# Kernel tuning notes

Hardware: AMD Instinct MI355X
Metric: run time of the kernel (lower is better)

Reference implementation:

```python
import jax, jax.numpy as jnp
import numpy as np

B, S, D, H = 2, 2048, 2048, 16
HD = D // H          # head_dim = 128
FF = 8192            # intermediate_size
LN_EPS = 1e-05
BIT_EPS = 1e-05


def _rope_tables(seq_len, head_dim):
    inv_freq = 1.0 / (10000.0 ** (np.arange(0, head_dim, 2, dtype=np.float64) / head_dim))
    ang = np.arange(seq_len, dtype=np.float64)[:, None] * inv_freq[None, :]  # [S, HD/2]
    ang = np.concatenate([ang, ang], axis=-1)  # [S, HD]
    return jnp.asarray(np.cos(ang), jnp.float32), jnp.asarray(np.sin(ang), jnp.float32)


def setup_inputs() -> dict:
    key = jax.random.key(0)
    ks = jax.random.split(key, 9)
    hidden_states = jax.random.normal(ks[0], (B, S, D), jnp.float32)
    # causal additive mask [1, S, S]
    causal = jnp.tril(jnp.ones((S, S), bool))
    attention_mask = jnp.where(causal, 0.0, -1e9)[None].astype(jnp.float32)
    cos, sin = _rope_tables(S, HD)
    w = lambda k, o, i: jax.random.normal(k, (o, i), jnp.float32) * 0.02
    return {
        'hidden_states': hidden_states,
        'attention_mask': attention_mask,
        'cos': cos, 'sin': sin,
        'wq': w(ks[1], D, D), 'wk': w(ks[2], D, D),
        'wv': w(ks[3], D, D), 'wo': w(ks[4], D, D),
        'wg': w(ks[5], FF, D), 'wu': w(ks[6], FF, D), 'wd': w(ks[7], D, FF),
        'ln1_w': jnp.ones((D,), jnp.float32),
        'ln2_w': jnp.ones((D,), jnp.float32),
    }


def bitlinear(x, w):
    # ternarize: clamp(round(w / (mean|w| + eps)), -1, 1); int8 cast in torch
    # breaks grad through the ternary values -> stop_gradient here.
    scale = jnp.mean(jnp.abs(w))
    tern = jax.lax.stop_gradient(jnp.clip(jnp.round(w / (scale + BIT_EPS)), -1.0, 1.0))
    # dequant = ternary * mean|w|, then standard linear (x @ W^T)
    return jnp.einsum('bsi,oi->bso', x, tern * scale)


def rmsnorm(x, w, eps=LN_EPS):
    var = jnp.mean(jnp.square(x.astype(jnp.float32)), axis=-1, keepdims=True)
    return w * (x * jax.lax.rsqrt(var + eps))


def rotate_half(x):
    x1, x2 = jnp.split(x, 2, axis=-1)
    return jnp.concatenate([-x2, x1], axis=-1)


def apply_rope(q, k, cos, sin):
    # q, k: [B, S, D] -> per-head rope -> back to [B, S, D]
    qh = q.reshape(B, S, H, HD)
    kh = k.reshape(B, S, H, HD)
    c = cos[None, :, None, :]
    s = sin[None, :, None, :]
    qe = qh * c + rotate_half(qh) * s
    ke = kh * c + rotate_half(kh) * s
    return qe.reshape(B, S, D), ke.reshape(B, S, D)


def reference(hidden_states, attention_mask, cos, sin,
              wq, wk, wv, wo, wg, wu, wd, ln1_w, ln2_w):
    residual = hidden_states
    # --- attention block ---
    x = rmsnorm(hidden_states, ln1_w)
    q = bitlinear(x, wq)
    k = bitlinear(x, wk)
    v = bitlinear(x, wv)
    q, k = apply_rope(q, k, cos, sin)
    # NOTE: scores over FULL hidden dim (no head split), scaled by sqrt(head_dim),
    # exactly as in the original module.
    scores = jnp.einsum('bsd,btd->bst', q, k) / jnp.sqrt(jnp.float32(HD))
    scores = scores + attention_mask
    probs = jax.nn.softmax(scores, axis=-1)
    attn_out = jnp.einsum('bst,btd->bsd', probs, v)
    attn_out = bitlinear(attn_out, wo)
    h = residual + attn_out
    # --- MLP block ---
    residual = h
    y = rmsnorm(h, ln2_w)
    gated = bitlinear(y, wg) * bitlinear(y, wu)
    out = bitlinear(gated, wd)
    return residual + out
```

## Files before the change

### kernel.cpp

```cpp
#include <hip/hip_runtime.h>
#include <stdint.h>

#define DEV __device__ __forceinline__

typedef __attribute__((ext_vector_type(8))) short short8;
typedef __attribute__((ext_vector_type(8))) __bf16 bf16x8;
typedef __attribute__((ext_vector_type(4))) float f32x4;

DEV unsigned short f2bf(float f) {
  union { float f; unsigned int u; } v; v.f = f;
  unsigned int r = v.u + 0x7fffu + ((v.u >> 16) & 1u);
  return (unsigned short)(r >> 16);
}
DEV float bf2f(unsigned short h) {
  union { unsigned int u; float f; } v; v.u = ((unsigned int)h) << 16;
  return v.f;
}
DEV f32x4 mfma16(short8 a, short8 b, f32x4 c) {
  return __builtin_amdgcn_mfma_f32_16x16x32_bf16(
      __builtin_bit_cast(bf16x8, a), __builtin_bit_cast(bf16x8, b), c, 0, 0, 0);
}
DEV void gload_lds16(const void* g, void* lds) {
  __builtin_amdgcn_global_load_lds(
      (const __attribute__((address_space(1))) void*)g,
      (__attribute__((address_space(3))) void*)lds, 16, 0, 0);
}

struct MArgs {
  const float* src[7];
  unsigned short* dst[7];
  int n[7];
  int sidx[7];
};

__global__ __launch_bounds__(256) void absmean_partial_multi(
    MArgs a, float* __restrict__ partial) {
  const int m = blockIdx.y;
  const float4* w4 = (const float4*)a.src[m];
  const int n4 = a.n[m] >> 2;
  float s = 0.f;
  for (int i = blockIdx.x * 256 + threadIdx.x; i < n4; i += 1024 * 256) {
    float4 v = w4[i];
    s += fabsf(v.x) + fabsf(v.y) + fabsf(v.z) + fabsf(v.w);
  }
#pragma unroll
  for (int mm = 1; mm < 64; mm <<= 1) s += __shfl_xor(s, mm);
  __shared__ float red[4];
  if ((threadIdx.x & 63) == 0) red[threadIdx.x >> 6] = s;
  __syncthreads();
  if (threadIdx.x == 0)
    partial[m * 1024 + blockIdx.x] = red[0] + red[1] + red[2] + red[3];
}

__global__ __launch_bounds__(256) void absmean_final(
    const float* __restrict__ partial, float* __restrict__ scales) {
  __shared__ double red[256];
  const int m = blockIdx.x;
  double s = 0.0;
  for (int i = threadIdx.x; i < 1024; i += 256) s += (double)partial[m * 1024 + i];
  red[threadIdx.x] = s;
  __syncthreads();
  for (int t = 128; t > 0; t >>= 1) {
    if (threadIdx.x < t) red[threadIdx.x] += red[threadIdx.x + t];
    __syncthreads();
  }
  if (threadIdx.x == 0) {
    const long long cnt = (m < 4) ? 4194304ll : 16777216ll;
    scales[m] = (float)(red[0] / (double)cnt);
  }
}

__global__ __launch_bounds__(256) void quantize_multi(
    MArgs a, const float* __restrict__ scales) {
  const int m = blockIdx.y;
  const float sc = scales[a.sidx[m]];
  const float inv = 1.f / (sc + 1e-5f);
  const float4* src = (const float4*)a.src[m];
  ushort4* dst = (ushort4*)a.dst[m];
  const int n4 = a.n[m] >> 2;
  for (int i = blockIdx.x * 256 + threadIdx.x; i < n4; i += 2048 * 256) {
    float4 v = src[i];
    ushort4 o;
    o.x = f2bf(fminf(fmaxf(rintf(v.x * inv), -1.f), 1.f) * sc);
    o.y = f2bf(fminf(fmaxf(rintf(v.y * inv), -1.f), 1.f) * sc);
    o.z = f2bf(fminf(fmaxf(rintf(v.z * inv), -1.f), 1.f) * sc);
    o.w = f2bf(fminf(fmaxf(rintf(v.w * inv), -1.f), 1.f) * sc);
    dst[i] = o;
  }
}

__global__ __launch_bounds__(256) void rmsnorm_k(
    const float* __restrict__ x, const float* __restrict__ wt,
    unsigned short* __restrict__ out) {
  const long long t = blockIdx.x;
  const float* xr = x + t * 2048;
  const int i0 = threadIdx.x * 8;
  float4 a = *(const float4*)(xr + i0);
  float4 b = *(const float4*)(xr + i0 + 4);
  float ss = a.x * a.x + a.y * a.y + a.z * a.z + a.w * a.w +
             b.x * b.x + b.y * b.y + b.z * b.z + b.w * b.w;
#pragma unroll
  for (int m = 1; m < 64; m <<= 1) ss += __shfl_xor(ss, m);
  __shared__ float red[4];
  if ((threadIdx.x & 63) == 0) red[threadIdx.x >> 6] = ss;
  __syncthreads();
  float tot = red[0] + red[1] + red[2] + red[3];
  float rs = rsqrtf(tot * (1.f / 2048.f) + 1e-5f);
  float4 wa = *(const float4*)(wt + i0);
  float4 wb = *(const float4*)(wt + i0 + 4);
  ushort4 o1, o2;
  o1.x = f2bf(a.x * wa.x * rs); o1.y = f2bf(a.y * wa.y * rs);
  o1.z = f2bf(a.z * wa.z * rs); o1.w = f2bf(a.w * wa.w * rs);
  o2.x = f2bf(b.x * wb.x * rs); o2.y = f2bf(b.y * wb.y * rs);
  o2.z = f2bf(b.z * wb.z * rs); o2.w = f2bf(b.w * wb.w * rs);
  *(ushort4*)(out + t * 2048 + i0) = o1;
  *(ushort4*)(out + t * 2048 + i0 + 4) = o2;
}

__global__ __launch_bounds__(256) void combine_rms(
    const float* __restrict__ ep, const unsigned short* __restrict__ p,
    const float* __restrict__ wt, float* __restrict__ hout,
    unsigned short* __restrict__ yout) {
  const long long t = blockIdx.x;
  const int i0 = threadIdx.x * 8;
  const long long base = t * 2048 + i0;
  float4 e1 = *(const float4*)(ep + base);
  float4 e2 = *(const float4*)(ep + base + 4);
  short8 pa = *(const short8*)(p + base);
  short8 pb = *(const short8*)(p + 8388608 + base);
  const float e[8] = {e1.x, e1.y, e1.z, e1.w, e2.x, e2.y, e2.z, e2.w};
  float h[8];
#pragma unroll
  for (int i = 0; i < 8; ++i)
    h[i] = e[i] + bf2f((unsigned short)pa[i]) + bf2f((unsigned short)pb[i]);
  float4 h1 = {h[0], h[1], h[2], h[3]};
  float4 h2 = {h[4], h[5], h[6], h[7]};
  *(float4*)(hout + base) = h1;
  *(float4*)(hout + base + 4) = h2;
  float ss = 0.f;
#pragma unroll
  for (int i = 0; i < 8; ++i) ss += h[i] * h[i];
#pragma unroll
  for (int m = 1; m < 64; m <<= 1) ss += __shfl_xor(ss, m);
  __shared__ float red[4];
  if ((threadIdx.x & 63) == 0) red[threadIdx.x >> 6] = ss;
  __syncthreads();
  const float tot = red[0] + red[1] + red[2] + red[3];
  const float rs = rsqrtf(tot * (1.f / 2048.f) + 1e-5f);
  float4 wa = *(const float4*)(wt + i0);
  float4 wb = *(const float4*)(wt + i0 + 4);
  ushort4 o1, o2;
  o1.x = f2bf(h[0] * wa.x * rs); o1.y = f2bf(h[1] * wa.y * rs);
  o1.z = f2bf(h[2] * wa.z * rs); o1.w = f2bf(h[3] * wa.w * rs);
  o2.x = f2bf(h[4] * wb.x * rs); o2.y = f2bf(h[5] * wb.y * rs);
  o2.z = f2bf(h[6] * wb.z * rs); o2.w = f2bf(h[7] * wb.w * rs);
  *(ushort4*)(yout + base) = o1;
  *(ushort4*)(yout + base + 4) = o2;
}

__global__ __launch_bounds__(256) void combine2(
    const float* __restrict__ ep, const unsigned short* __restrict__ p,
    float* __restrict__ out) {
  const long long base = (long long)blockIdx.x * 2048 + threadIdx.x * 8;
  float4 e1 = *(const float4*)(ep + base);
  float4 e2 = *(const float4*)(ep + base + 4);
  short8 pa = *(const short8*)(p + base);
  short8 pb = *(const short8*)(p + 8388608 + base);
  float4 o1, o2;
  o1.x = e1.x + bf2f((unsigned short)pa[0]) + bf2f((unsigned short)pb[0]);
  o1.y = e1.y + bf2f((unsigned short)pa[1]) + bf2f((unsigned short)pb[1]);
  o1.z = e1.z + bf2f((unsigned short)pa[2]) + bf2f((unsigned short)pb[2]);
  o1.w = e1.w + bf2f((unsigned short)pa[3]) + bf2f((unsigned short)pb[3]);
  o2.x = e2.x + bf2f((unsigned short)pa[4]) + bf2f((unsigned short)pb[4]);
  o2.y = e2.y + bf2f((unsigned short)pa[5]) + bf2f((unsigned short)pb[5]);
  o2.z = e2.z + bf2f((unsigned short)pa[6]) + bf2f((unsigned short)pb[6]);
  o2.w = e2.w + bf2f((unsigned short)pa[7]) + bf2f((unsigned short)pb[7]);
  *(float4*)(out + base) = o1;
  *(float4*)(out + base + 4) = o2;
}

__global__ __launch_bounds__(256) void rope_k(
    const unsigned short* __restrict__ qkv, const float* __restrict__ cosT,
    const float* __restrict__ sinT, unsigned short* __restrict__ qr,
    unsigned short* __restrict__ kr) {
  const long long gid = (long long)blockIdx.x * 256 + threadIdx.x;
  const int t = (int)(gid >> 10);
  const int r = (int)(gid & 1023);
  const int h = r >> 6, d = r & 63;
  const int s = t & 2047;
  const unsigned short* row = qkv + (long long)t * 6144;
  const float c = cosT[s * 128 + d], sn = sinT[s * 128 + d];
  const int col = h * 128 + d;
  const float SC = 0.08838834764831845f;
  float q1 = bf2f(row[col]), q2 = bf2f(row[col + 64]);
  float k1 = bf2f(row[2048 + col]), k2 = bf2f(row[2048 + col + 64]);
  long long ob = (long long)t * 2048 + col;
  qr[ob] = f2bf((q1 * c - q2 * sn) * SC);
  qr[ob + 64] = f2bf((q2 * c + q1 * sn) * SC);
  kr[ob] = f2bf(k1 * c - k2 * sn);
  kr[ob + 64] = f2bf(k2 * c + k1 * sn);
}

__global__ __launch_bounds__(256) void vtrans_k(
    const unsigned short* __restrict__ qkv, unsigned short* __restrict__ vt) {
  __shared__ unsigned short tile[64][66];
  const int tt = blockIdx.x << 6, dd = blockIdx.y << 6;
  const long long b = blockIdx.z;
  const int r0 = threadIdx.x >> 4, c0 = (threadIdx.x & 15) << 2;
#pragma unroll
  for (int i = 0; i < 4; ++i) {
    const int row = r0 + i * 16;
    ushort4 v = *(const ushort4*)&qkv[(b * 2048 + tt + row) * 6144 + 4096 + dd + c0];
    tile[row][c0] = v.x; tile[row][c0 + 1] = v.y;
    tile[row][c0 + 2] = v.z; tile[row][c0 + 3] = v.w;
  }
  __syncthreads();
#pragma unroll
  for (int i = 0; i < 4; ++i) {
    const int d = r0 + i * 16;
    ushort4 o;
    o.x = tile[c0][d]; o.y = tile[c0 + 1][d];
    o.z = tile[c0 + 2][d]; o.w = tile[c0 + 3][d];
    *(ushort4*)&vt[(b * 2048 + dd + d) * 2048 + tt + c0] = o;
  }
}

__global__ __launch_bounds__(256) void softmax_causal(
    const float* __restrict__ scores, unsigned short* __restrict__ probs) {
  const int r = blockIdx.x;
  const int s = r & 2047;
  const float* src = scores + (long long)r * 2048;
  unsigned short* dst = probs + (long long)r * 2048;
  const int L = s + 1;
  const int j0 = threadIdx.x * 8;
  float4 a = *(const float4*)(src + j0);
  float4 b = *(const float4*)(src + j0 + 4);
  float v[8] = {a.x, a.y, a.z, a.w, b.x, b.y, b.z, b.w};
  float mx = -1e30f;
#pragma unroll
  for (int i = 0; i < 8; ++i) {
    if (j0 + i >= L) v[i] = -1e30f;
    mx = fmaxf(mx, v[i]);
  }
#pragma unroll
  for (int m = 1; m < 64; m <<= 1) mx = fmaxf(mx, __shfl_xor(mx, m));
  __shared__ float redM[4], redS[4];
  if ((threadIdx.x & 63) == 0) redM[threadIdx.x >> 6] = mx;
  __syncthreads();
  mx = fmaxf(fmaxf(redM[0], redM[1]), fmaxf(redM[2], redM[3]));
  float sum = 0.f;
#pragma unroll
  for (int i = 0; i < 8; ++i) {
    v[i] = (j0 + i < L) ? __expf(v[i] - mx) : 0.f;
    sum += v[i];
  }
#pragma unroll
  for (int m = 1; m < 64; m <<= 1) sum += __shfl_xor(sum, m);
  if ((threadIdx.x & 63) == 0) redS[threadIdx.x >> 6] = sum;
  __syncthreads();
  const float inv = 1.f / (redS[0] + redS[1] + redS[2] + redS[3]);
  ushort4 o1, o2;
  o1.x = f2bf(v[0] * inv); o1.y = f2bf(v[1] * inv);
  o1.z = f2bf(v[2] * inv); o1.w = f2bf(v[3] * inv);
  o2.x = f2bf(v[4] * inv); o2.y = f2bf(v[5] * inv);
  o2.z = f2bf(v[6] * inv); o2.w = f2bf(v[7] * inv);
  *(ushort4*)(dst + j0) = o1;
  *(ushort4*)(dst + j0 + 4) = o2;
}

template <int EPI, int CAUSAL>
__global__ __launch_bounds__(256) void gemm_nt(
    const unsigned short* __restrict__ A, const unsigned short* __restrict__ Bw,
    void* __restrict__ Cp, int M, int N, int K,
    long long sAz, long long sBz, long long sCz) {
  const long long m0 = (long long)blockIdx.y * 128;
  const long long n0 = (long long)blockIdx.x * 128;
  if (CAUSAL == 1 && n0 > m0 + 127) return;
  __shared__ __align__(16) unsigned short sA[2][128 * 32];
  __shared__ __align__(16) unsigned short sB[2][128 * 32];
  const int tid = threadIdx.x;
  const int w = tid >> 6, l = tid & 63;
  const long long z = blockIdx.z;
  A += z * sAz;
  Bw += z * sBz;
  const long long cofs = z * sCz;
  const int wr = w >> 1, wc = w & 1;
  const int lrow = l & 15;
  const int rj = ((l >> 4) ^ ((l >> 1) & 3)) << 4;

  f32x4 acc[4][4] = {};
  int nk = K >> 5;
  if (CAUSAL == 2) nk = (int)((m0 + 128) >> 5);
  int cur = 0;

  auto stage = [&](int buf, int k0) {
#pragma unroll
    for (int i = 0; i < 2; ++i) {
      const int flat = (w * 2 + i) * 64 + l;
      const int row = flat >> 2;
      const int col = ((flat & 3) ^ ((row >> 1) & 3)) * 8;
      gload_lds16(&A[(m0 + row) * K + k0 + col], (char*)&sA[buf][0] + (w * 2 + i) * 1024);
      gload_lds16(&Bw[(n0 + row) * K + k0 + col], (char*)&sB[buf][0] + (w * 2 + i) * 1024);
    }
  };

  stage(0, 0);
  __syncthreads();
  for (int kt = 0; kt < nk; ++kt) {
    if (kt + 1 < nk) stage(cur ^ 1, (kt + 1) << 5);
    short8 af[4], bfr[4];
#pragma unroll
    for (int m = 0; m < 4; ++m)
      af[m] = *(const short8*)((char*)&sA[cur][0] + (wr * 64 + m * 16 + lrow) * 64 + rj);
#pragma unroll
    for (int n = 0; n < 4; ++n)
      bfr[n] = *(const short8*)((char*)&sB[cur][0] + (wc * 64 + n * 16 + lrow) * 64 + rj);
#pragma unroll
    for (int m = 0; m < 4; ++m)
#pragma unroll
      for (int n = 0; n < 4; ++n)
        acc[m][n] = mfma16(af[m], bfr[n], acc[m][n]);
    __syncthreads();
    cur ^= 1;
  }

  const int orow = (l >> 4) * 4, ocol = l & 15;
#pragma unroll
  for (int m = 0; m < 4; ++m)
#pragma unroll
    for (int n = 0; n < 4; ++n)
#pragma unroll
      for (int r = 0; r < 4; ++r) {
        long long gr = m0 + wr * 64 + m * 16 + orow + r;
        long long gc = n0 + wc * 64 + n * 16 + ocol;
        long long idx = cofs + gr * N + gc;
        float v = acc[m][n][r];
        if (EPI == 0) ((unsigned short*)Cp)[idx] = f2bf(v);
        else ((float*)Cp)[idx] = v;
      }
}

template <int EPI>
__global__ __launch_bounds__(512, 2) void gemm256(
    const unsigned short* __restrict__ A, const unsigned short* __restrict__ Bw,
    void* __restrict__ Cp, const void* __restrict__ Ep,
    int N, int K, int nbx, int kLen, int ng,
    long long sAz, long long sBz, long long zCout) {
  __shared__ __align__(16) unsigned short lds[4 * 2 * 8192];
  __shared__ __align__(16) unsigned short ldsDummy[512];
  const int tid = threadIdx.x;
  const int wid = tid >> 6, l = tid & 63;
  const int wr = wid >> 2, wcn = wid & 3;

  const int nwg = gridDim.x;
  const int q8 = nwg >> 3;
  const int lin = (blockIdx.x & 7) * q8 + (blockIdx.x >> 3);
  const int t32 = lin >> 5, r32 = lin & 31;
  const int tpr = nbx >> 3;
  const int tm = t32 / tpr, tn = t32 - tm * tpr;
  const long long m0 = (long long)(tm * 4 + (r32 >> 3)) * 256;
  const long long n0 = (long long)(tn * 8 + (r32 & 7)) * 256;
  const int z = blockIdx.z;
  A += z * sAz;
  Bw += z * sBz;
  const long long kbase = (long long)z * kLen;
  const long long zofs = (long long)z * zCout;

  const int stRow = (l >> 2);
  const int stCol = (((l & 3) ^ ((l >> 3) & 3))) * 8;
  auto stage = [&](int chunk, int sslot) {
    if (chunk < ng) {
      char* base = (char*)lds + (sslot * 2) * 16384;
      const long long kcol = kbase + (long long)chunk * 32 + stCol;
#pragma unroll
      for (int i = 0; i < 2; ++i) {
        const int row = (wid * 2 + i) * 16 + stRow;
        gload_lds16(&A[(m0 + row) * K + kcol], base + (wid * 2 + i) * 1024);
        gload_lds16(&Bw[(n0 + row) * K + kcol],
                    base + 16384 + (wid * 2 + i) * 1024);
      }
    } else {
#pragma unroll
      for (int i = 0; i < 4; ++i) gload_lds16(&A[m0 * K], (char*)ldsDummy);
    }
  };

  const int ar = l & 15;
  const int rj = ((l >> 4) ^ ((l >> 1) & 3)) << 4;
  const int aoff = (wr * 128 + ar) * 64 + rj;
  const int boff = (wcn * 64 + ar) * 64 + rj;

  f32x4 acc[8][4] = {};
  short8 aX[4], bX[4], aY[4], bY[4];

  stage(0, 0); stage(1, 1); stage(2, 2);
  asm volatile("s_waitcnt vmcnt(4)" ::: "memory");
  __builtin_amdgcn_s_barrier();
#pragma unroll
  for (int m = 0; m < 4; ++m)
    aX[m] = *(const short8*)((const char*)lds + aoff + m * 1024);
#pragma unroll
  for (int n = 0; n < 4; ++n)
    bX[n] = *(const short8*)((const char*)lds + 16384 + boff + n * 1024);

#define CHUNK_BODY(SLOT, NSLOT, SYNC, cur03, curB, nxt03, nxtB, cc)            \
  {                                                                            \
    const char* sAc = (const char*)lds + (SLOT * 2) * 16384;                   \
    const char* sAn = (const char*)lds + (NSLOT * 2) * 16384;                  \
    const char* sBn = (const char*)lds + (NSLOT * 2 + 1) * 16384;              \
    short8 a47[4];                                                             \
    _Pragma("unroll") for (int m = 0; m < 4; ++m)                              \
        a47[m] = *(const short8*)(sAc + aoff + 4096 + m * 1024);               \
    stage((cc) + 3, (SLOT + 3) & 3);                                           \
    __builtin_amdgcn_s_setprio(1);                                             \
    _Pragma("unroll") for (int m = 0; m < 4; ++m)                              \
      _Pragma("unroll") for (int n = 0; n < 4; ++n)                            \
          acc[m][n] = mfma16(cur03[m], curB[n], acc[m][n]);                    \
    __builtin_amdgcn_s_setprio(0);                                             \
    if (SYNC) {                                                                \
      asm volatile("s_waitcnt vmcnt(4)" ::: "memory");                         \
      __builtin_amdgcn_s_barrier();                                            \
    }                                                                          \
    _Pragma("unroll") for (int m = 0; m < 4; ++m)                              \
        nxt03[m] = *(const short8*)(sAn + aoff + m * 1024);                    \
    _Pragma("unroll") for (int n = 0; n < 4; ++n)                              \
        nxtB[n] = *(const short8*)(sBn + boff + n * 1024);                     \
    __builtin_amdgcn_s_setprio(1);                                             \
    _Pragma("unroll") for (int m = 0; m < 4; ++m)                              \
      _Pragma("unroll") for (int n = 0; n < 4; ++n)                            \
          acc[m + 4][n] = mfma16(a47[m], curB[n], acc[m + 4][n]);              \
    __builtin_amdgcn_s_setprio(0);                                             \
  }

  for (int c = 0; c < ng; c += 4) {
    CHUNK_BODY(0, 1, false, aX, bX, aY, bY, c);
    CHUNK_BODY(1, 2, true, aY, bY, aX, bX, c + 1);
    CHUNK_BODY(2, 3, false, aX, bX, aY, bY, c + 2);
    CHUNK_BODY(3, 0, true, aY, bY, aX, bX, c + 3);
  }
#undef CHUNK_BODY
  asm volatile("s_waitcnt vmcnt(0)" ::: "memory");
  __builtin_amdgcn_s_barrier();

  const int orow = (l >> 4) * 4, ocol = l & 15;
#pragma unroll
  for (int m = 0; m < 8; ++m)
#pragma unroll
    for (int n = 0; n < 4; ++n)
#pragma unroll
      for (int r = 0; r < 4; ++r) {
        const long long gr = m0 + wr * 128 + m * 16 + orow + r;
        const long long gc = n0 + wcn * 64 + n * 16 + ocol;
        const long long idx = zofs + gr * N + gc;
        const float v = acc[m][n][r];
        if (EPI == 0) {
          ((unsigned short*)Cp)[idx] = f2bf(v);
        } else if (EPI == 2) {
          ((unsigned short*)Cp)[idx] = f2bf(bf2f(((const unsigned short*)Ep)[idx]) * v);
        } else {
          ((float*)Cp)[idx] = v;
        }
      }
}

extern "C" void kernel_launch(void* const* d_in, const int* in_sizes, int n_in,
                              void* d_out, int out_size, void* d_ws, size_t ws_size,
                              hipStream_t stream) {
  (void)in_sizes; (void)n_in; (void)out_size; (void)ws_size;
  const float* hidden = (const float*)d_in[0];
  const float* cosT = (const float*)d_in[2];
  const float* sinT = (const float*)d_in[3];
  const float* wq = (const float*)d_in[4];
  const float* wk = (const float*)d_in[5];
  const float* wv = (const float*)d_in[6];
  const float* wo = (const float*)d_in[7];
  const float* wg = (const float*)d_in[8];
  const float* wu = (const float*)d_in[9];
  const float* wd = (const float*)d_in[10];
  const float* ln1 = (const float*)d_in[11];
  const float* ln2 = (const float*)d_in[12];

  const size_t MB = 1ull << 20;
  char* ws = (char*)d_ws;
  unsigned short* xn    = (unsigned short*)(ws + 0);
  unsigned short* wqkvq = (unsigned short*)(ws + 16 * MB);
  unsigned short* qkv   = (unsigned short*)(ws + 40 * MB);
  unsigned short* qrb   = (unsigned short*)(ws + 88 * MB);
  unsigned short* krb   = (unsigned short*)(ws + 104 * MB);
  unsigned short* vtb   = (unsigned short*)(ws + 120 * MB);
  float*          scoresB = (float*)(ws + 0);
  unsigned short* probsB  = (unsigned short*)(ws + 40 * MB);
  unsigned short* partb = (unsigned short*)(ws + 0);
  unsigned short* wgq   = (unsigned short*)(ws + 0);
  unsigned short* wuq   = (unsigned short*)(ws + 32 * MB);
  unsigned short* gbuf  = (unsigned short*)(ws + 64 * MB);
  unsigned short* attnb = (unsigned short*)(ws + 136 * MB);
  unsigned short* woq   = (unsigned short*)(ws + 152 * MB);
  float*          hbuf  = (float*)(ws + 160 * MB);
  unsigned short* ybuf  = (unsigned short*)(ws + 192 * MB);
  unsigned short* gated = (unsigned short*)(ws + 208 * MB);
  unsigned short* wdq   = (unsigned short*)(ws + 272 * MB);
  float* wspart         = (float*)(ws + 304 * MB);
  float* scales         = (float*)(ws + 304 * MB + 32768);

  MArgs am;
  am.src[0] = wq; am.src[1] = wk; am.src[2] = wv; am.src[3] = wo;
  am.src[4] = wg; am.src[5] = wu; am.src[6] = wd;
  am.n[0] = am.n[1] = am.n[2] = am.n[3] = 4194304;
  am.n[4] = am.n[5] = am.n[6] = 16777216;
  for (int i = 0; i < 7; ++i) { am.dst[i] = nullptr; am.sidx[i] = i; }
  absmean_partial_multi<<<dim3(1024, 7), 256, 0, stream>>>(am, wspart);
  absmean_final<<<7, 256, 0, stream>>>(wspart, scales);

  MArgs qe;
  qe.src[0] = wq; qe.dst[0] = wqkvq;            qe.n[0] = 4194304;  qe.sidx[0] = 0;
  qe.src[1] = wk; qe.dst[1] = wqkvq + 4194304;  qe.n[1] = 4194304;  qe.sidx[1] = 1;
  qe.src[2] = wv; qe.dst[2] = wqkvq + 8388608;  qe.n[2] = 4194304;  qe.sidx[2] = 2;
  qe.src[3] = wo; qe.dst[3] = woq;              qe.n[3] = 4194304;  qe.sidx[3] = 3;
  qe.src[4] = wd; qe.dst[4] = wdq;              qe.n[4] = 16777216; qe.sidx[4] = 6;
  qe.src[5] = wq; qe.dst[5] = nullptr; qe.n[5] = 0; qe.sidx[5] = 0;
  qe.src[6] = wq; qe.dst[6] = nullptr; qe.n[6] = 0; qe.sidx[6] = 0;
  quantize_multi<<<dim3(2048, 5), 256, 0, stream>>>(qe, scales);

  rmsnorm_k<<<4096, 256, 0, stream>>>(hidden, ln1, xn);

  gemm256<0><<<dim3(384, 1, 1), 512, 0, stream>>>(
      xn, wqkvq, qkv, nullptr, 6144, 2048, 24, 2048, 64, 0, 0, 0);

  rope_k<<<16384, 256, 0, stream>>>(qkv, cosT, sinT, qrb, krb);
  vtrans_k<<<dim3(32, 32, 2), 256, 0, stream>>>(qkv, vtb);

  gemm_nt<4, 1><<<dim3(16, 16, 2), 256, 0, stream>>>(
      qrb, krb, scoresB, 2048, 2048, 2048, 4194304, 4194304, 4194304);
  softmax_causal<<<4096, 256, 0, stream>>>(scoresB, probsB);
  gemm_nt<0, 2><<<dim3(16, 16, 2), 256, 0, stream>>>(
      probsB, vtb, attnb, 2048, 2048, 2048, 4194304, 4194304, 4194304);

  gemm256<0><<<dim3(128, 1, 2), 512, 0, stream>>>(
      attnb, woq, partb, nullptr, 2048, 2048, 8, 1024, 32, 0, 0, 8388608);
  combine_rms<<<4096, 256, 0, stream>>>(hidden, partb, ln2, hbuf, ybuf);

  MArgs ql;
  ql.src[0] = wg; ql.dst[0] = wgq; ql.n[0] = 16777216; ql.sidx[0] = 4;
  ql.src[1] = wu; ql.dst[1] = wuq; ql.n[1] = 16777216; ql.sidx[1] = 5;
  for (int i = 2; i < 7; ++i) { ql.src[i] = wg; ql.dst[i] = nullptr; ql.n[i] = 0; ql.sidx[i] = 0; }
  quantize_multi<<<dim3(2048, 2), 256, 0, stream>>>(ql, scales);

  gemm256<0><<<dim3(512, 1, 1), 512, 0, stream>>>(
      ybuf, wgq, gbuf, nullptr, 8192, 2048, 32, 2048, 64, 0, 0, 0);
  gemm256<2><<<dim3(512, 1, 1), 512, 0, stream>>>(
      ybuf, wuq, gated, gbuf, 8192, 2048, 32, 2048, 64, 0, 0, 0);

  gemm256<0><<<dim3(128, 1, 2), 512, 0, stream>>>(
      gated, wdq, partb, nullptr, 2048, 8192, 8, 4096, 128, 0, 0, 8388608);
  combine2<<<4096, 256, 0, stream>>>(hbuf, partb, (float*)d_out);
}
```

Baseline: 770.1 us.

## Fuse gate/up GEMMs into one dual-B kernel and split-K the QKV projection

Adds a gemm_gu kernel that loads each A tile once and multiplies it against both the gate and up weight tiles, writing the gated product directly. This removes the separate gate buffer round-trip and the second read of the activations. The QKV GEMM now uses split-K across two partial buffers, which rope and the V-transpose sum as they read, so more blocks are launched. Quantization of wd moves next to wg/wu, and the workspace layout is reshuffled to fit. The new kernel carries twice the accumulators per thread, so register pressure is a risk, and the split-K partial sums add extra traffic into rope and vtrans.

After: 930.7 us. 20.9% more time.

```diff
diff --git a/kernel.cpp b/kernel.cpp
--- a/kernel.cpp
+++ b/kernel.cpp
@@ -180,7 +180,7 @@
 }
 
 __global__ __launch_bounds__(256) void rope_k(
-    const unsigned short* __restrict__ qkv, const float* __restrict__ cosT,
+    const unsigned short* __restrict__ p, const float* __restrict__ cosT,
     const float* __restrict__ sinT, unsigned short* __restrict__ qr,
     unsigned short* __restrict__ kr) {
   const long long gid = (long long)blockIdx.x * 256 + threadIdx.x;
@@ -188,12 +188,15 @@
   const int r = (int)(gid & 1023);
   const int h = r >> 6, d = r & 63;
   const int s = t & 2047;
-  const unsigned short* row = qkv + (long long)t * 6144;
+  const unsigned short* r0 = p + (long long)t * 6144;
+  const unsigned short* r1 = r0 + 25165824;
   const float c = cosT[s * 128 + d], sn = sinT[s * 128 + d];
   const int col = h * 128 + d;
   const float SC = 0.08838834764831845f;
-  float q1 = bf2f(row[col]), q2 = bf2f(row[col + 64]);
-  float k1 = bf2f(row[2048 + col]), k2 = bf2f(row[2048 + col + 64]);
+  float q1 = bf2f(r0[col]) + bf2f(r1[col]);
+  float q2 = bf2f(r0[col + 64]) + bf2f(r1[col + 64]);
+  float k1 = bf2f(r0[2048 + col]) + bf2f(r1[2048 + col]);
+  float k2 = bf2f(r0[2048 + col + 64]) + bf2f(r1[2048 + col + 64]);
   long long ob = (long long)t * 2048 + col;
   qr[ob] = f2bf((q1 * c - q2 * sn) * SC);
   qr[ob + 64] = f2bf((q2 * c + q1 * sn) * SC);
@@ -202,7 +205,7 @@
 }
 
 __global__ __launch_bounds__(256) void vtrans_k(
-    const unsigned short* __restrict__ qkv, unsigned short* __restrict__ vt) {
+    const unsigned short* __restrict__ p, unsigned short* __restrict__ vt) {
   __shared__ unsigned short tile[64][66];
   const int tt = blockIdx.x << 6, dd = blockIdx.y << 6;
   const long long b = blockIdx.z;
@@ -210,9 +213,13 @@
 #pragma unroll
   for (int i = 0; i < 4; ++i) {
     const int row = r0 + i * 16;
-    ushort4 v = *(const ushort4*)&qkv[(b * 2048 + tt + row) * 6144 + 4096 + dd + c0];
-    tile[row][c0] = v.x; tile[row][c0 + 1] = v.y;
-    tile[row][c0 + 2] = v.z; tile[row][c0 + 3] = v.w;
+    const long long src = (b * 2048 + tt + row) * 6144 + 4096 + dd + c0;
+    ushort4 v0 = *(const ushort4*)&p[src];
+    ushort4 v1 = *(const ushort4*)&p[25165824 + src];
+    tile[row][c0] = f2bf(bf2f(v0.x) + bf2f(v1.x));
+    tile[row][c0 + 1] = f2bf(bf2f(v0.y) + bf2f(v1.y));
+    tile[row][c0 + 2] = f2bf(bf2f(v0.z) + bf2f(v1.z));
+    tile[row][c0 + 3] = f2bf(bf2f(v0.w) + bf2f(v1.w));
   }
   __syncthreads();
 #pragma unroll
@@ -463,6 +470,123 @@
       }
 }
 
+__global__ __launch_bounds__(512, 2) void gemm_gu(
+    const unsigned short* __restrict__ A, const unsigned short* __restrict__ Bg,
+    const unsigned short* __restrict__ Bu, unsigned short* __restrict__ Cp,
+    int ng) {
+  const int K = 2048;
+  __shared__ __align__(16) unsigned short lds[4 * 16384];
+  __shared__ __align__(16) unsigned short ldsDummy[512];
+  const int tid = threadIdx.x;
+  const int wid = tid >> 6, l = tid & 63;
+  const int wr = wid >> 2, wcn = wid & 3;
+
+  const int lin = (blockIdx.x & 7) * 128 + (blockIdx.x >> 3);
+  const int t32 = lin >> 5, r32 = lin & 31;
+  const int tm = t32 >> 3, tn = t32 & 7;
+  const long long m0 = (long long)(tm * 4 + (r32 >> 3)) * 256;
+  const long long n0 = (long long)(tn * 8 + (r32 & 7)) * 128;
+
+  const int stRow = l >> 2;
+  const int stCol = (((l & 3) ^ ((l >> 3) & 3))) * 8;
+  const int rowB = tid >> 2;
+  const int colB = ((tid & 3) ^ ((rowB >> 1) & 3)) * 8;
+  auto stage = [&](int chunk, int sslot) {
+    if (chunk < ng) {
+      char* base = (char*)lds + sslot * 32768;
+      const long long kc = (long long)chunk * 32;
+#pragma unroll
+      for (int i = 0; i < 2; ++i) {
+        const int row = (wid * 2 + i) * 16 + stRow;
+        gload_lds16(&A[(m0 + row) * K + kc + stCol], base + (wid * 2 + i) * 1024);
+      }
+      gload_lds16(&Bg[(n0 + rowB) * K + kc + colB], base + 16384 + wid * 1024);
+      gload_lds16(&Bu[(n0 + rowB) * K + kc + colB], base + 24576 + wid * 1024);
+    } else {
+#pragma unroll
+      for (int i = 0; i < 4; ++i) gload_lds16(&A[m0 * K], (char*)ldsDummy);
+    }
+  };
+
+  const int ar = l & 15;
+  const int rj = ((l >> 4) ^ ((l >> 1) & 3)) << 4;
+  const int aoff = (wr * 128 + ar) * 64 + rj;
+  const int bgoff = 16384 + (wcn * 32 + ar) * 64 + rj;
+  const int buoff = 24576 + (wcn * 32 + ar) * 64 + rj;
+
+  f32x4 accg[8][2] = {}, accu[8][2] = {};
+  short8 aX[4], gX[2], uX[2], aY[4], gY[2], uY[2];
+
+  stage(0, 0); stage(1, 1); stage(2, 2);
+  asm volatile("s_waitcnt vmcnt(4)" ::: "memory");
+  __builtin_amdgcn_s_barrier();
+#pragma unroll
+  for (int m = 0; m < 4; ++m)
+    aX[m] = *(const short8*)((const char*)lds + aoff + m * 1024);
+#pragma unroll
+  for (int n = 0; n < 2; ++n) {
+    gX[n] = *(const short8*)((const char*)lds + bgoff + n * 1024);
+    uX[n] = *(const short8*)((const char*)lds + buoff + n * 1024);
+  }
+
+#define GU_BODY(SLOT, NSLOT, SYNC, cA, cG, cU, nA, nG, nU, cc)                 \
+  {                                                                            \
+    const char* sC = (const char*)lds + SLOT * 32768;                          \
+    const char* sN = (const char*)lds + NSLOT * 32768;                         \
+    short8 a47[4];                                                             \
+    _Pragma("unroll") for (int m = 0; m < 4; ++m)                              \
+        a47[m] = *(const short8*)(sC + aoff + 4096 + m * 1024);                \
+    stage((cc) + 3, (SLOT + 3) & 3);                                           \
+    __builtin_amdgcn_s_setprio(1);                                             \
+    _Pragma("unroll") for (int m = 0; m < 4; ++m)                              \
+      _Pragma("unroll") for (int n = 0; n < 2; ++n) {                          \
+        accg[m][n] = mfma16(cA[m], cG[n], accg[m][n]);                         \
+        accu[m][n] = mfma16(cA[m], cU[n], accu[m][n]);                         \
+      }                                                                        \
+    __builtin_amdgcn_s_setprio(0);                                             \
+    if (SYNC) {                                                                \
+      asm volatile("s_waitcnt vmcnt(4)" ::: "memory");                         \
+      __builtin_amdgcn_s_barrier();                                            \
+    }                                                                          \
+    _Pragma("unroll") for (int m = 0; m < 4; ++m)                              \
+        nA[m] = *(const short8*)(sN + aoff + m * 1024);                        \
+    _Pragma("unroll") for (int n = 0; n < 2; ++n) {                            \
+      nG[n] = *(const short8*)(sN + bgoff + n * 1024);                         \
+      nU[n] = *(const short8*)(sN + buoff + n * 1024);                         \
+    }                                                                          \
+    __builtin_amdgcn_s_setprio(1);                                             \
+    _Pragma("unroll") for (int m = 0; m < 4; ++m)                              \
+      _Pragma("unroll") for (int n = 0; n < 2; ++n) {                          \
+        accg[m + 4][n] = mfma16(a47[m], cG[n], accg[m + 4][n]);                \
+        accu[m + 4][n] = mfma16(a47[m], cU[n], accu[m + 4][n]);                \
+      }                                                                        \
+    __builtin_amdgcn_s_setprio(0);                                             \
+  }
+
+  for (int c = 0; c < ng; c += 4) {
+    GU_BODY(0, 1, false, aX, gX, uX, aY, gY, uY, c);
+    GU_BODY(1, 2, true, aY, gY, uY, aX, gX, uX, c + 1);
+    GU_BODY(2, 3, false, aX, gX, uX, aY, gY, uY, c + 2);
+    GU_BODY(3, 0, true, aY, gY, uY, aX, gX, uX, c + 3);
+  }
+#undef GU_BODY
+  asm volatile("s_waitcnt vmcnt(0)" ::: "memory");
+  __builtin_amdgcn_s_barrier();
+
+  const int orow = (l >> 4) * 4, ocol = l & 15;
+#pragma unroll
+  for (int m = 0; m < 8; ++m)
+#pragma unroll
+    for (int n = 0; n < 2; ++n)
+#pragma unroll
+      for (int r = 0; r < 4; ++r) {
+        const long long gr = m0 + wr * 128 + m * 16 + orow + r;
+        const long long gc = n0 + wcn * 32 + n * 16 + ocol;
+        const float gv = bf2f(f2bf(accg[m][n][r]));
+        Cp[gr * 8192 + gc] = f2bf(gv * accu[m][n][r]);
+      }
+}
+
 extern "C" void kernel_launch(void* const* d_in, const int* in_sizes, int n_in,
                               void* d_out, int out_size, void* d_ws, size_t ws_size,
                               hipStream_t stream) {
@@ -484,24 +608,24 @@
   char* ws = (char*)d_ws;
   unsigned short* xn    = (unsigned short*)(ws + 0);
   unsigned short* wqkvq = (unsigned short*)(ws + 16 * MB);
-  unsigned short* qkv   = (unsigned short*)(ws + 40 * MB);
-  unsigned short* qrb   = (unsigned short*)(ws + 88 * MB);
-  unsigned short* krb   = (unsigned short*)(ws + 104 * MB);
-  unsigned short* vtb   = (unsigned short*)(ws + 120 * MB);
+  unsigned short* qkvp  = (unsigned short*)(ws + 40 * MB);
+  unsigned short* qrb   = (unsigned short*)(ws + 136 * MB);
+  unsigned short* krb   = (unsigned short*)(ws + 152 * MB);
+  unsigned short* vtb   = (unsigned short*)(ws + 168 * MB);
+  unsigned short* woq   = (unsigned short*)(ws + 184 * MB);
+  float*          hbuf  = (float*)(ws + 192 * MB);
+  unsigned short* ybuf  = (unsigned short*)(ws + 224 * MB);
   float*          scoresB = (float*)(ws + 0);
   unsigned short* probsB  = (unsigned short*)(ws + 40 * MB);
-  unsigned short* partb = (unsigned short*)(ws + 0);
+  unsigned short* attnb   = (unsigned short*)(ws + 56 * MB);
+  unsigned short* partbO  = (unsigned short*)(ws + 80 * MB);
   unsigned short* wgq   = (unsigned short*)(ws + 0);
   unsigned short* wuq   = (unsigned short*)(ws + 32 * MB);
-  unsigned short* gbuf  = (unsigned short*)(ws + 64 * MB);
-  unsigned short* attnb = (unsigned short*)(ws + 136 * MB);
-  unsigned short* woq   = (unsigned short*)(ws + 152 * MB);
-  float*          hbuf  = (float*)(ws + 160 * MB);
-  unsigned short* ybuf  = (unsigned short*)(ws + 192 * MB);
-  unsigned short* gated = (unsigned short*)(ws + 208 * MB);
-  unsigned short* wdq   = (unsigned short*)(ws + 272 * MB);
-  float* wspart         = (float*)(ws + 304 * MB);
-  float* scales         = (float*)(ws + 304 * MB + 32768);
+  unsigned short* gated = (unsigned short*)(ws + 64 * MB);
+  unsigned short* wdq   = (unsigned short*)(ws + 128 * MB);
+  unsigned short* partbD = (unsigned short*)(ws + 160 * MB);
+  float* wspart         = (float*)(ws + 240 * MB);
+  float* scales         = (float*)(ws + 240 * MB + 32768);
 
   MArgs am;
   am.src[0] = wq; am.src[1] = wk; am.src[2] = wv; am.src[3] = wo;
@@ -513,22 +637,20 @@
   absmean_final<<<7, 256, 0, stream>>>(wspart, scales);
 
   MArgs qe;
-  qe.src[0] = wq; qe.dst[0] = wqkvq;            qe.n[0] = 4194304;  qe.sidx[0] = 0;
-  qe.src[1] = wk; qe.dst[1] = wqkvq + 4194304;  qe.n[1] = 4194304;  qe.sidx[1] = 1;
-  qe.src[2] = wv; qe.dst[2] = wqkvq + 8388608;  qe.n[2] = 4194304;  qe.sidx[2] = 2;
-  qe.src[3] = wo; qe.dst[3] = woq;              qe.n[3] = 4194304;  qe.sidx[3] = 3;
-  qe.src[4] = wd; qe.dst[4] = wdq;              qe.n[4] = 16777216; qe.sidx[4] = 6;
-  qe.src[5] = wq; qe.dst[5] = nullptr; qe.n[5] = 0; qe.sidx[5] = 0;
-  qe.src[6] = wq; qe.dst[6] = nullptr; qe.n[6] = 0; qe.sidx[6] = 0;
-  quantize_multi<<<dim3(2048, 5), 256, 0, stream>>>(qe, scales);
+  qe.src[0] = wq; qe.dst[0] = wqkvq;            qe.n[0] = 4194304; qe.sidx[0] = 0;
+  qe.src[1] = wk; qe.dst[1] = wqkvq + 4194304;  qe.n[1] = 4194304; qe.sidx[1] = 1;
+  qe.src[2] = wv; qe.dst[2] = wqkvq + 8388608;  qe.n[2] = 4194304; qe.sidx[2] = 2;
+  qe.src[3] = wo; qe.dst[3] = woq;              qe.n[3] = 4194304; qe.sidx[3] = 3;
+  for (int i = 4; i < 7; ++i) { qe.src[i] = wq; qe.dst[i] = nullptr; qe.n[i] = 0; qe.sidx[i] = 0; }
+  quantize_multi<<<dim3(2048, 4), 256, 0, stream>>>(qe, scales);
 
   rmsnorm_k<<<4096, 256, 0, stream>>>(hidden, ln1, xn);
 
-  gemm256<0><<<dim3(384, 1, 1), 512, 0, stream>>>(
-      xn, wqkvq, qkv, nullptr, 6144, 2048, 24, 2048, 64, 0, 0, 0);
-
-  rope_k<<<16384, 256, 0, stream>>>(qkv, cosT, sinT, qrb, krb);
-  vtrans_k<<<dim3(32, 32, 2), 256, 0, stream>>>(qkv, vtb);
+  gemm256<0><<<dim3(384, 1, 2), 512, 0, stream>>>(
+      xn, wqkvq, qkvp, nullptr, 6144, 2048, 24, 1024, 32, 0, 0, 25165824);
+
+  rope_k<<<16384, 256, 0, stream>>>(qkvp, cosT, sinT, qrb, krb);
+  vtrans_k<<<dim3(32, 32, 2), 256, 0, stream>>>(qkvp, vtb);
 
   gemm_nt<4, 1><<<dim3(16, 16, 2), 256, 0, stream>>>(
       qrb, krb, scoresB, 2048, 2048, 2048, 4194304, 4194304, 4194304);
@@ -537,21 +659,19 @@
       probsB, vtb, attnb, 2048, 2048, 2048, 4194304, 4194304, 4194304);
 
   gemm256<0><<<dim3(128, 1, 2), 512, 0, stream>>>(
-      attnb, woq, partb, nullptr, 2048, 2048, 8, 1024, 32, 0, 0, 8388608);
-  combine_rms<<<4096, 256, 0, stream>>>(hidden, partb, ln2, hbuf, ybuf);
+      attnb, woq, partbO, nullptr, 2048, 2048, 8, 1024, 32, 0, 0, 8388608);
+  combine_rms<<<4096, 256, 0, stream>>>(hidden, partbO, ln2, hbuf, ybuf);
 
   MArgs ql;
   ql.src[0] = wg; ql.dst[0] = wgq; ql.n[0] = 16777216; ql.sidx[0] = 4;
   ql.src[1] = wu; ql.dst[1] = wuq; ql.n[1] = 16777216; ql.sidx[1] = 5;
-  for (int i = 2; i < 7; ++i) { ql.src[i] = wg; ql.dst[i] = nullptr; ql.n[i] = 0; ql.sidx[i] = 0; }
-  quantize_multi<<<dim3(2048, 2), 256, 0, stream>>>(ql, scales);
-
-  gemm256<0><<<dim3(512, 1, 1), 512, 0, stream>>>(
-      ybuf, wgq, gbuf, nullptr, 8192, 2048, 32, 2048, 64, 0, 0, 0);
-  gemm256<2><<<dim3(512, 1, 1), 512, 0, stream>>>(
-      ybuf, wuq, gated, gbuf, 8192, 2048, 32, 2048, 64, 0, 0, 0);
+  ql.src[2] = wd; ql.dst[2] = wdq; ql.n[2] = 16777216; ql.sidx[2] = 6;
+  for (int i = 3; i < 7; ++i) { ql.src[i] = wg; ql.dst[i] = nullptr; ql.n[i] = 0; ql.sidx[i] = 0; }
+  quantize_multi<<<dim3(2048, 3), 256, 0, stream>>>(ql, scales);
+
+  gemm_gu<<<dim3(1024, 1, 1), 512, 0, stream>>>(ybuf, wgq, wuq, gated, 64);
 
   gemm256<0><<<dim3(128, 1, 2), 512, 0, stream>>>(
-      gated, wdq, partb, nullptr, 2048, 8192, 8, 4096, 128, 0, 0, 8388608);
-  combine2<<<4096, 256, 0, stream>>>(hbuf, partb, (float*)d_out);
-}
+      gated, wdq, partbD, nullptr, 2048, 8192, 8, 4096, 128, 0, 0, 8388608);
+  combine2<<<4096, 256, 0, stream>>>(hbuf, partbD, (float*)d_out);
+}
```

## Split-K the QKV projection and fold partial sums into rope and V transpose

Applied to the files above, without the earlier changes.

The QKV GEMM now runs as a two-way split-K grid (z=2), writing two bf16 partial outputs, which doubles the number of workgroups for better CU occupancy. The rope and V-transpose kernels sum the two partials while reading, so no separate combine pass is needed. The wd quantization moves later to sit with the wg/wu quantization, and the workspace layout is reshuffled to fit the larger partial buffer. The cost is twice the QKV output traffic, plus an extra rounding step because the partials are stored in bf16 before being summed.

Result: slower. 794.7 us (+3.2%).

```diff
diff --git a/kernel.cpp b/kernel.cpp
--- a/kernel.cpp
+++ b/kernel.cpp
@@ -180,7 +180,7 @@
 }
 
 __global__ __launch_bounds__(256) void rope_k(
-    const unsigned short* __restrict__ qkv, const float* __restrict__ cosT,
+    const unsigned short* __restrict__ p, const float* __restrict__ cosT,
     const float* __restrict__ sinT, unsigned short* __restrict__ qr,
     unsigned short* __restrict__ kr) {
   const long long gid = (long long)blockIdx.x * 256 + threadIdx.x;
@@ -188,12 +188,15 @@
   const int r = (int)(gid & 1023);
   const int h = r >> 6, d = r & 63;
   const int s = t & 2047;
-  const unsigned short* row = qkv + (long long)t * 6144;
+  const unsigned short* r0 = p + (long long)t * 6144;
+  const unsigned short* r1 = r0 + 25165824;
   const float c = cosT[s * 128 + d], sn = sinT[s * 128 + d];
   const int col = h * 128 + d;
   const float SC = 0.08838834764831845f;
-  float q1 = bf2f(row[col]), q2 = bf2f(row[col + 64]);
-  float k1 = bf2f(row[2048 + col]), k2 = bf2f(row[2048 + col + 64]);
+  float q1 = bf2f(r0[col]) + bf2f(r1[col]);
+  float q2 = bf2f(r0[col + 64]) + bf2f(r1[col + 64]);
+  float k1 = bf2f(r0[2048 + col]) + bf2f(r1[2048 + col]);
+  float k2 = bf2f(r0[2048 + col + 64]) + bf2f(r1[2048 + col + 64]);
   long long ob = (long long)t * 2048 + col;
   qr[ob] = f2bf((q1 * c - q2 * sn) * SC);
   qr[ob + 64] = f2bf((q2 * c + q1 * sn) * SC);
@@ -202,7 +205,7 @@
 }
 
 __global__ __launch_bounds__(256) void vtrans_k(
-    const unsigned short* __restrict__ qkv, unsigned short* __restrict__ vt) {
+    const unsigned short* __restrict__ p, unsigned short* __restrict__ vt) {
   __shared__ unsigned short tile[64][66];
   const int tt = blockIdx.x << 6, dd = blockIdx.y << 6;
   const long long b = blockIdx.z;
@@ -210,9 +213,13 @@
 #pragma unroll
   for (int i = 0; i < 4; ++i) {
     const int row = r0 + i * 16;
-    ushort4 v = *(const ushort4*)&qkv[(b * 2048 + tt + row) * 6144 + 4096 + dd + c0];
-    tile[row][c0] = v.x; tile[row][c0 + 1] = v.y;
-    tile[row][c0 + 2] = v.z; tile[row][c0 + 3] = v.w;
+    const long long src = (b * 2048 + tt + row) * 6144 + 4096 + dd + c0;
+    ushort4 v0 = *(const ushort4*)&p[src];
+    ushort4 v1 = *(const ushort4*)&p[25165824 + src];
+    tile[row][c0] = f2bf(bf2f(v0.x) + bf2f(v1.x));
+    tile[row][c0 + 1] = f2bf(bf2f(v0.y) + bf2f(v1.y));
+    tile[row][c0 + 2] = f2bf(bf2f(v0.z) + bf2f(v1.z));
+    tile[row][c0 + 3] = f2bf(bf2f(v0.w) + bf2f(v1.w));
   }
   __syncthreads();
 #pragma unroll
@@ -484,22 +491,23 @@
   char* ws = (char*)d_ws;
   unsigned short* xn    = (unsigned short*)(ws + 0);
   unsigned short* wqkvq = (unsigned short*)(ws + 16 * MB);
-  unsigned short* qkv   = (unsigned short*)(ws + 40 * MB);
-  unsigned short* qrb   = (unsigned short*)(ws + 88 * MB);
-  unsigned short* krb   = (unsigned short*)(ws + 104 * MB);
-  unsigned short* vtb   = (unsigned short*)(ws + 120 * MB);
+  unsigned short* qkvp  = (unsigned short*)(ws + 40 * MB);
+  unsigned short* qrb   = (unsigned short*)(ws + 136 * MB);
+  unsigned short* krb   = (unsigned short*)(ws + 152 * MB);
+  unsigned short* vtb   = (unsigned short*)(ws + 168 * MB);
+  unsigned short* woq   = (unsigned short*)(ws + 184 * MB);
+  float*          hbuf  = (float*)(ws + 192 * MB);
+  unsigned short* ybuf  = (unsigned short*)(ws + 224 * MB);
   float*          scoresB = (float*)(ws + 0);
   unsigned short* probsB  = (unsigned short*)(ws + 40 * MB);
-  unsigned short* partb = (unsigned short*)(ws + 0);
+  unsigned short* attnb   = (unsigned short*)(ws + 56 * MB);
+  unsigned short* partbO  = (unsigned short*)(ws + 80 * MB);
   unsigned short* wgq   = (unsigned short*)(ws + 0);
   unsigned short* wuq   = (unsigned short*)(ws + 32 * MB);
   unsigned short* gbuf  = (unsigned short*)(ws + 64 * MB);
-  unsigned short* attnb = (unsigned short*)(ws + 136 * MB);
-  unsigned short* woq   = (unsigned short*)(ws + 152 * MB);
-  float*          hbuf  = (float*)(ws + 160 * MB);
-  unsigned short* ybuf  = (unsigned short*)(ws + 192 * MB);
-  unsigned short* gated = (unsigned short*)(ws + 208 * MB);
-  unsigned short* wdq   = (unsigned short*)(ws + 272 * MB);
+  unsigned short* gated = (unsigned short*)(ws + 128 * MB);
+  unsigned short* wdq   = (unsigned short*)(ws + 240 * MB);
+  unsigned short* partbD = (unsigned short*)(ws + 272 * MB);
   float* wspart         = (float*)(ws + 304 * MB);
   float* scales         = (float*)(ws + 304 * MB + 32768);
 
@@ -513,22 +521,20 @@
   absmean_final<<<7, 256, 0, stream>>>(wspart, scales);
 
   MArgs qe;
-  qe.src[0] = wq; qe.dst[0] = wqkvq;            qe.n[0] = 4194304;  qe.sidx[0] = 0;
-  qe.src[1] = wk; qe.dst[1] = wqkvq + 4194304;  qe.n[1] = 4194304;  qe.sidx[1] = 1;
-  qe.src[2] = wv; qe.dst[2] = wqkvq + 8388608;  qe.n[2] = 4194304;  qe.sidx[2] = 2;
-  qe.src[3] = wo; qe.dst[3] = woq;              qe.n[3] = 4194304;  qe.sidx[3] = 3;
-  qe.src[4] = wd; qe.dst[4] = wdq;              qe.n[4] = 16777216; qe.sidx[4] = 6;
-  qe.src[5] = wq; qe.dst[5] = nullptr; qe.n[5] = 0; qe.sidx[5] = 0;
-  qe.src[6] = wq; qe.dst[6] = nullptr; qe.n[6] = 0; qe.sidx[6] = 0;
-  quantize_multi<<<dim3(2048, 5), 256, 0, stream>>>(qe, scales);
+  qe.src[0] = wq; qe.dst[0] = wqkvq;            qe.n[0] = 4194304; qe.sidx[0] = 0;
+  qe.src[1] = wk; qe.dst[1] = wqkvq + 4194304;  qe.n[1] = 4194304; qe.sidx[1] = 1;
+  qe.src[2] = wv; qe.dst[2] = wqkvq + 8388608;  qe.n[2] = 4194304; qe.sidx[2] = 2;
+  qe.src[3] = wo; qe.dst[3] = woq;              qe.n[3] = 4194304; qe.sidx[3] = 3;
+  for (int i = 4; i < 7; ++i) { qe.src[i] = wq; qe.dst[i] = nullptr; qe.n[i] = 0; qe.sidx[i] = 0; }
+  quantize_multi<<<dim3(2048, 4), 256, 0, stream>>>(qe, scales);
 
   rmsnorm_k<<<4096, 256, 0, stream>>>(hidden, ln1, xn);
 
-  gemm256<0><<<dim3(384, 1, 1), 512, 0, stream>>>(
-      xn, wqkvq, qkv, nullptr, 6144, 2048, 24, 2048, 64, 0, 0, 0);
-
-  rope_k<<<16384, 256, 0, stream>>>(qkv, cosT, sinT, qrb, krb);
-  vtrans_k<<<dim3(32, 32, 2), 256, 0, stream>>>(qkv, vtb);
+  gemm256<0><<<dim3(384, 1, 2), 512, 0, stream>>>(
+      xn, wqkvq, qkvp, nullptr, 6144, 2048, 24, 1024, 32, 0, 0, 25165824);
+
+  rope_k<<<16384, 256, 0, stream>>>(qkvp, cosT, sinT, qrb, krb);
+  vtrans_k<<<dim3(32, 32, 2), 256, 0, stream>>>(qkvp, vtb);
 
   gemm_nt<4, 1><<<dim3(16, 16, 2), 256, 0, stream>>>(
       qrb, krb, scoresB, 2048, 2048, 2048, 4194304, 4194304, 4194304);
@@ -537,14 +543,15 @@
       probsB, vtb, attnb, 2048, 2048, 2048, 4194304, 4194304, 4194304);
 
   gemm256<0><<<dim3(128, 1, 2), 512, 0, stream>>>(
-      attnb, woq, partb, nullptr, 2048, 2048, 8, 1024, 32, 0, 0, 8388608);
-  combine_rms<<<4096, 256, 0, stream>>>(hidden, partb, ln2, hbuf, ybuf);
+      attnb, woq, partbO, nullptr, 2048, 2048, 8, 1024, 32, 0, 0, 8388608);
+  combine_rms<<<4096, 256, 0, stream>>>(hidden, partbO, ln2, hbuf, ybuf);
 
   MArgs ql;
   ql.src[0] = wg; ql.dst[0] = wgq; ql.n[0] = 16777216; ql.sidx[0] = 4;
   ql.src[1] = wu; ql.dst[1] = wuq; ql.n[1] = 16777216; ql.sidx[1] = 5;
-  for (int i = 2; i < 7; ++i) { ql.src[i] = wg; ql.dst[i] = nullptr; ql.n[i] = 0; ql.sidx[i] = 0; }
-  quantize_multi<<<dim3(2048, 2), 256, 0, stream>>>(ql, scales);
+  ql.src[2] = wd; ql.dst[2] = wdq; ql.n[2] = 16777216; ql.sidx[2] = 6;
+  for (int i = 3; i < 7; ++i) { ql.src[i] = wg; ql.dst[i] = nullptr; ql.n[i] = 0; ql.sidx[i] = 0; }
+  quantize_multi<<<dim3(2048, 3), 256, 0, stream>>>(ql, scales);
 
   gemm256<0><<<dim3(512, 1, 1), 512, 0, stream>>>(
       ybuf, wgq, gbuf, nullptr, 8192, 2048, 32, 2048, 64, 0, 0, 0);
@@ -552,6 +559,6 @@
       ybuf, wuq, gated, gbuf, 8192, 2048, 32, 2048, 64, 0, 0, 0);
 
   gemm256<0><<<dim3(128, 1, 2), 512, 0, stream>>>(
-      gated, wdq, partb, nullptr, 2048, 8192, 8, 4096, 128, 0, 0, 8388608);
-  combine2<<<4096, 256, 0, stream>>>(hbuf, partb, (float*)d_out);
-}
+      gated, wdq, partbD, nullptr, 2048, 8192, 8, 4096, 128, 0, 0, 8388608);
+  combine2<<<4096, 256, 0, stream>>>(hbuf, partbD, (float*)d_out);
+}
```
